# Performance work log

Measured on AMD Instinct MI355X. Metric: run time of the kernel, lower is better.

## Reference

```python
import jax, jax.numpy as jnp
import numpy as np

HIDDEN = 4096
NUM_HEADS = 32
NUM_KV_HEADS = 8
HEAD_DIM = HIDDEN // NUM_HEADS  # 128
Q_SIZE = NUM_HEADS * HEAD_DIM    # 4096
KV_SIZE = NUM_KV_HEADS * HEAD_DIM  # 1024
SCALE = 1.0 / HEAD_DIM  # attention_multiplier=None -> head_dim ** (-1)
ROPE_BASE = 10000.0


def _rope_neox(x, positions):
    # x: [B, S, H, D], positions: [B, S] int
    half = HEAD_DIM // 2
    inv_freq = 1.0 / (ROPE_BASE ** (jnp.arange(0, half, dtype=jnp.float32) / half))
    freqs = positions.astype(jnp.float32)[..., None] * inv_freq  # [B, S, half]
    cos = jnp.cos(freqs)[:, :, None, :]  # [B, S, 1, half]
    sin = jnp.sin(freqs)[:, :, None, :]
    x1, x2 = x[..., :half], x[..., half:]
    return jnp.concatenate([x1 * cos - x2 * sin, x2 * cos + x1 * sin], axis=-1)


def setup_inputs() -> dict:
    key = jax.random.key(0)
    k1, k2, k3 = jax.random.split(key, 3)
    B, S = 2, 2048
    positions = jnp.broadcast_to(jnp.arange(S, dtype=jnp.int32), (B, S))
    hidden_states = jax.random.normal(k1, (B, S, HIDDEN), dtype=jnp.float32) * 0.02
    w_qkv = jax.random.normal(k2, (Q_SIZE + 2 * KV_SIZE, HIDDEN), dtype=jnp.float32) * 0.02
    w_o = jax.random.normal(k3, (HIDDEN, Q_SIZE), dtype=jnp.float32) * 0.02
    return {"positions": positions, "hidden_states": hidden_states, "w_qkv": w_qkv, "w_o": w_o}


def reference(positions, hidden_states, w_qkv, w_o):
    B, S, _ = hidden_states.shape
    # fused QKV projection
    qkv = jnp.einsum('bsh,oh->bso', hidden_states, w_qkv)
    q = qkv[..., :Q_SIZE].reshape(B, S, NUM_HEADS, HEAD_DIM)
    k = qkv[..., Q_SIZE:Q_SIZE + KV_SIZE].reshape(B, S, NUM_KV_HEADS, HEAD_DIM)
    v = qkv[..., Q_SIZE + KV_SIZE:].reshape(B, S, NUM_KV_HEADS, HEAD_DIM)
    # neox-style RoPE on q and k
    q = _rope_neox(q, positions)
    k = _rope_neox(k, positions)
    # GQA: repeat kv heads
    rep = NUM_HEADS // NUM_KV_HEADS
    k = jnp.repeat(k, rep, axis=2)  # [B, S, NUM_HEADS, D]
    v = jnp.repeat(v, rep, axis=2)
    # causal attention
    scores = jnp.einsum('bqhd,bkhd->bhqk', q, k) * SCALE
    causal = jnp.tril(jnp.ones((S, S), dtype=bool))
    scores = jnp.where(causal, scores, jnp.finfo(scores.dtype).min)
    probs = jax.nn.softmax(scores, axis=-1)
    attn = jnp.einsum('bhqk,bkhd->bqhd', probs, v).reshape(B, S, Q_SIZE)
    # output projection
    return jnp.einsum('bsq,hq->bsh', attn, w_o)
```

## Files before the change

kernel.cpp:

```cpp
#include <hip/hip_runtime.h>
#include <hip/hip_bf16.h>
#include <cmath>

typedef __bf16 bf16x8 __attribute__((ext_vector_type(8)));
typedef __bf16 bf16x4 __attribute__((ext_vector_type(4)));
typedef float  f32x4  __attribute__((ext_vector_type(4)));
typedef unsigned int u32;
typedef u32 u32x4 __attribute__((ext_vector_type(4)));

#define AS1 __attribute__((address_space(1)))
#define AS3 __attribute__((address_space(3)))
#define GLDS16(gp, lp) __builtin_amdgcn_global_load_lds((AS1 void*)(gp), (AS3 void*)(lp), 16, 0, 0)

#define B_DIM 2
#define S_LEN 2048
#define HIDDEN 4096
#define NHEADS 32
#define NKV 8
#define HDIM 128
#define QSZ 4096
#define KVSZ 1024
#define QKVSZ 6144
#define GK 4096
#define ATT_SCALE 0.0078125f
#define L2E 1.4426950408889634f

__global__ __launch_bounds__(256) void conv_f32_bf16(const float* __restrict__ in,
                                                     __bf16* __restrict__ out, int n4) {
    int idx = blockIdx.x * 256 + threadIdx.x;
    if (idx < n4) {
        float4 v = ((const float4*)in)[idx];
        bf16x4 o;
        o[0] = (__bf16)v.x; o[1] = (__bf16)v.y; o[2] = (__bf16)v.z; o[3] = (__bf16)v.w;
        ((bf16x4*)out)[idx] = o;
    }
}

__global__ __launch_bounds__(256) void rope_table_kernel(float* __restrict__ ct,
                                                         float* __restrict__ st) {
    int idx = blockIdx.x * 256 + threadIdx.x;
    int p = idx >> 6, i = idx & 63;
    float inv = expf(-(float)i * (9.210340371976184f / 64.0f));
    float freq = (float)p * inv;
    float s, c;
    sincosf(freq, &s, &c);
    ct[idx] = c; st[idx] = s;
}

template<typename OUT>
__global__ __launch_bounds__(512, 2) void gemm256(const __bf16* __restrict__ A,
                                                  const __bf16* __restrict__ B,
                                                  OUT* __restrict__ C,
                                                  int N) {
    __shared__ __bf16 Asm[2 * 16384 + 2 * 16384];
    char* Bbase = (char*)Asm + 65536;

    const int tid = threadIdx.x;
    const int w = tid >> 6, l = tid & 63;
    const int l15 = l & 15, l4 = l >> 4;
    const int wr = w >> 2, wc = w & 3;

    const int nwg = gridDim.x * gridDim.y;
    const int orig = blockIdx.y * gridDim.x + blockIdx.x;
    const int swz = (orig & 7) * (nwg >> 3) + (orig >> 3);
    const int bx = swz % gridDim.x, by = swz / gridDim.x;
    const int m0 = by * 256, n0 = bx * 256;

    const __bf16* Ag = A + (size_t)m0 * GK;
    const __bf16* Bg = B + (size_t)n0 * GK;

#define STAGE_AQ(q, tile) do {                                                  \
        int c_ = (q) * 512 + tid;                                               \
        int r_ = c_ >> 3;                                                       \
        int jg_ = (tid & 7) ^ (r_ & 7);                                         \
        GLDS16(Ag + (size_t)r_ * GK + (tile) * 64 + jg_ * 8,                    \
               (char*)Asm + ((tile) & 1) * 32768 + c_ * 16);                    \
    } while (0)
#define STAGE_BS(s, tile) do {                                                  \
        _Pragma("unroll")                                                       \
        for (int i_ = 0; i_ < 2; ++i_) {                                        \
            int v_ = i_ * 512 + tid;                                            \
            int r_ = (v_ >> 8) * 64 + (s) * 32 + ((v_ >> 3) & 31);              \
            int jg_ = (v_ & 7) ^ (r_ & 7);                                      \
            int c_ = r_ * 8 + (v_ & 7);                                         \
            GLDS16(Bg + (size_t)r_ * GK + (tile) * 64 + jg_ * 8,                \
                   Bbase + ((tile) & 1) * 32768 + c_ * 16);                     \
        }                                                                       \
    } while (0)

#define LOAD_A(DST, MH) do {                                                    \
        _Pragma("unroll")                                                       \
        for (int m2 = 0; m2 < 4; ++m2) {                                        \
            int row = wr * 128 + ((MH) * 4 + m2) * 16 + l15;                    \
            _Pragma("unroll")                                                   \
            for (int kk = 0; kk < 2; ++kk) {                                    \
                int j = (kk * 4 + l4) ^ (row & 7);                              \
                DST[m2][kk] = *(const bf16x8*)(Als + row * 64 + j * 8);         \
            }                                                                   \
        }                                                                       \
    } while (0)
#define LOAD_B(DST, NH) do {                                                    \
        _Pragma("unroll")                                                       \
        for (int n2 = 0; n2 < 2; ++n2) {                                        \
            int row = wc * 64 + ((NH) * 2 + n2) * 16 + l15;                     \
            _Pragma("unroll")                                                   \
            for (int kk = 0; kk < 2; ++kk) {                                    \
                int j = (kk * 4 + l4) ^ (row & 7);                              \
                DST[n2][kk] = *(const bf16x8*)(Bls + row * 64 + j * 8);         \
            }                                                                   \
        }                                                                       \
    } while (0)
#define MFMA_QUAD(AF, BF, MI0, NI0)                                             \
    _Pragma("unroll")                                                           \
    for (int m2 = 0; m2 < 4; ++m2)                                              \
        _Pragma("unroll")                                                       \
        for (int n2 = 0; n2 < 2; ++n2)                                          \
            _Pragma("unroll")                                                   \
            for (int kk = 0; kk < 2; ++kk)                                      \
                acc[(MI0) + m2][(NI0) + n2] =                                   \
                    __builtin_amdgcn_mfma_f32_16x16x32_bf16(                    \
                        AF[m2][kk], BF[n2][kk], acc[(MI0) + m2][(NI0) + n2], 0, 0, 0);
#define PH_SYNC_PRE  do { __builtin_amdgcn_sched_barrier(0);                    \
        __builtin_amdgcn_s_barrier();                                           \
        asm volatile("s_waitcnt lgkmcnt(0)" ::: "memory");                      \
        __builtin_amdgcn_sched_barrier(0); } while (0)
#define PH_SYNC_POST do { __builtin_amdgcn_sched_barrier(0);                    \
        __builtin_amdgcn_s_barrier(); } while (0)

    f32x4 acc[8][4] = {};

    const int T = GK / 64;
    STAGE_AQ(0, 0); STAGE_AQ(1, 0); STAGE_AQ(2, 0); STAGE_AQ(3, 0);
    STAGE_BS(0, 0); STAGE_BS(1, 0);
    STAGE_AQ(0, 1); STAGE_AQ(2, 1); STAGE_BS(0, 1);
    asm volatile("s_waitcnt vmcnt(4)" ::: "memory");
    __builtin_amdgcn_s_barrier();

    for (int t = 0; t < T; ++t) {
        const __bf16* Als = Asm + (t & 1) * 16384;
        const __bf16* Bls = (__bf16*)Bbase + (t & 1) * 16384;
        bf16x8 af0[4][2], af1[4][2], bfr[2][2];
        LOAD_A(af0, 0);
        LOAD_B(bfr, 0);
        if (t + 1 < T) { STAGE_AQ(1, t + 1); STAGE_AQ(3, t + 1); }
        PH_SYNC_PRE;
        __builtin_amdgcn_s_setprio(1);
        MFMA_QUAD(af0, bfr, 0, 0);
        __builtin_amdgcn_s_setprio(0);
        PH_SYNC_POST;
        LOAD_B(bfr, 1);
        if (t + 1 < T) STAGE_BS(1, t + 1);
        PH_SYNC_PRE;
        __builtin_amdgcn_s_setprio(1);
        MFMA_QUAD(af0, bfr, 0, 2);
        __builtin_amdgcn_s_setprio(0);
        PH_SYNC_POST;
        LOAD_A(af1, 1);
        LOAD_B(bfr, 0);
        if (t + 2 < T) { STAGE_AQ(0, t + 2); STAGE_AQ(2, t + 2); }
        PH_SYNC_PRE;
        __builtin_amdgcn_s_setprio(1);
        MFMA_QUAD(af1, bfr, 4, 0);
        __builtin_amdgcn_s_setprio(0);
        PH_SYNC_POST;
        LOAD_B(bfr, 1);
        if (t + 2 < T) STAGE_BS(0, t + 2);
        PH_SYNC_PRE;
        __builtin_amdgcn_s_setprio(1);
        MFMA_QUAD(af1, bfr, 4, 2);
        __builtin_amdgcn_s_setprio(0);
        if (t + 2 < T)      { asm volatile("s_waitcnt vmcnt(4)" ::: "memory"); }
        else if (t + 1 < T) { asm volatile("s_waitcnt vmcnt(0)" ::: "memory"); }
        PH_SYNC_POST;
    }
#undef PH_SYNC_PRE
#undef PH_SYNC_POST
#undef MFMA_QUAD
#undef LOAD_A
#undef LOAD_B
#undef STAGE_AQ
#undef STAGE_BS

#pragma unroll
    for (int mi = 0; mi < 8; ++mi)
#pragma unroll
        for (int ni = 0; ni < 4; ++ni)
#pragma unroll
            for (int r = 0; r < 4; ++r)
                C[(size_t)(m0 + wr * 128 + mi * 16 + l4 * 4 + r) * N
                  + n0 + wc * 64 + ni * 16 + l15] = (OUT)acc[mi][ni][r];
}

__global__ __launch_bounds__(256) void rope_kernel(const __bf16* __restrict__ qkv,
                                                   const int* __restrict__ pos,
                                                   const float* __restrict__ ct,
                                                   const float* __restrict__ st,
                                                   __bf16* __restrict__ Qb,
                                                   __bf16* __restrict__ Kb) {
    const int tid = threadIdx.x;
    const int tok = blockIdx.x;
    const int b = tok >> 11, s = tok & 2047;
    const int p = pos[tok];
    const __bf16* base = qkv + (size_t)tok * QKVSZ;
    const float* cb = ct + (size_t)p * 64;
    const float* sb = st + (size_t)p * 64;
    for (int idx = tid; idx < 2560; idx += 256) {
        int head = idx >> 6, i = idx & 63;
        float c = cb[i], sn = sb[i];
        if (head < 32) {
            float x1 = (float)base[head * HDIM + i];
            float x2 = (float)base[head * HDIM + 64 + i];
            size_t o = ((size_t)(b * 32 + head) * S_LEN + s) * HDIM + i;
            Qb[o]      = (__bf16)((x1 * c - x2 * sn) * ATT_SCALE);
            Qb[o + 64] = (__bf16)((x2 * c + x1 * sn) * ATT_SCALE);
        } else {
            int g = head - 32;
            float x1 = (float)base[QSZ + g * HDIM + i];
            float x2 = (float)base[QSZ + g * HDIM + 64 + i];
            size_t o = ((size_t)(b * 8 + g) * S_LEN + s) * HDIM + i;
            Kb[o]      = (__bf16)(x1 * c - x2 * sn);
            Kb[o + 64] = (__bf16)(x2 * c + x1 * sn);
        }
    }
}

__global__ __launch_bounds__(256) void vtrans_kernel(const __bf16* __restrict__ qkv,
                                                     __bf16* __restrict__ Vt) {
    __shared__ __bf16 T[64][132];
    const int tid = threadIdx.x;
    const int st = blockIdx.x, g = blockIdx.y, b = blockIdx.z;
    const __bf16* src = qkv + ((size_t)(b * S_LEN + st * 64)) * QKVSZ + (QSZ + KVSZ) + g * HDIM;
#pragma unroll
    for (int it = 0; it < 8; ++it) {
        int c = it * 256 + tid;
        int row = c >> 5;
        int c4 = c & 31;
        bf16x4 v = *(const bf16x4*)(src + (size_t)row * QKVSZ + c4 * 4);
        *(bf16x4*)(&T[row][c4 * 4]) = v;
    }
    __syncthreads();
#pragma unroll
    for (int it = 0; it < 8; ++it) {
        int c = it * 256 + tid;
        int d = c >> 4;
        int s4 = (c & 15) * 4;
        bf16x4 o;
        o[0] = T[s4 + 0][d]; o[1] = T[s4 + 1][d]; o[2] = T[s4 + 2][d]; o[3] = T[s4 + 3][d];
        *(bf16x4*)(Vt + ((size_t)(b * 8 + g) * HDIM + d) * S_LEN + st * 64 + s4) = o;
    }
}

__global__ __launch_bounds__(512, 2) void attn_kernel(const __bf16* __restrict__ Q,
                                                      const __bf16* __restrict__ K,
                                                      const __bf16* __restrict__ Vt,
                                                      __bf16* __restrict__ O) {
    const int tid = threadIdx.x;
    const int w = tid >> 6, l = tid & 63;
    const int l15 = l & 15, l4 = l >> 4;
    const int flat = blockIdx.x + (blockIdx.y << 3) + (blockIdx.z << 8);
    const int swz = (flat & 7) * 64 + (flat >> 3);
    const int qt = swz & 7;
    const int hb = swz >> 3;
    const int h = hb & 31, b = hb >> 5;
    const int g = h >> 2;
    const int qw0 = qt * 256 + w * 32;

    __shared__ __bf16 Ks[4][64 * 128];
    __shared__ __bf16 Vs[4][128 * 64];

    const __bf16* Qp = Q + ((size_t)((b * 32 + h) * S_LEN + qw0)) * HDIM;
    const __bf16* Kp = K + (size_t)(b * 8 + g) * S_LEN * HDIM;
    const __bf16* Vp = Vt + (size_t)(b * 8 + g) * HDIM * S_LEN;

    bf16x8 qf[2][4];
#pragma unroll
    for (int qh = 0; qh < 2; ++qh)
#pragma unroll
        for (int kk = 0; kk < 4; ++kk)
            qf[qh][kk] = *(const bf16x8*)(Qp + (size_t)(qh * 16 + l15) * HDIM + kk * 32 + l4 * 8);

    f32x4 acc[2][8] = {};
    float m[2]    = {-1e30f, -1e30f};
    float lsum[2] = {0.f, 0.f};

#define RED16(x, OPINS) do {                                                      \
        u32 ra_ = __builtin_bit_cast(u32, x), rb_;                                \
        asm("v_mov_b32 %0, %1" : "=v"(rb_) : "v"(ra_));                           \
        asm("v_permlane16_swap_b32 %0, %1" : "+v"(ra_), "+v"(rb_));               \
        x = OPINS(__builtin_bit_cast(float, ra_), __builtin_bit_cast(float, rb_));\
    } while (0)
#define RED32(x, OPINS) do {                                                      \
        u32 ra_ = __builtin_bit_cast(u32, x), rb_;                                \
        asm("v_mov_b32 %0, %1" : "=v"(rb_) : "v"(ra_));                           \
        asm("v_permlane32_swap_b32 %0, %1" : "+v"(ra_), "+v"(rb_));               \
        x = OPINS(__builtin_bit_cast(float, ra_), __builtin_bit_cast(float, rb_));\
    } while (0)
#define FADD_(a_, b_) ((a_) + (b_))

#define STAGE(ktile) do {                                                          \
        const int buf_ = (ktile) & 3;                                              \
        const __bf16* kbase = Kp + (size_t)(ktile) * 64 * HDIM;                    \
        _Pragma("unroll")                                                          \
        for (int i_ = 0; i_ < 2; ++i_) {                                           \
            int c_ = i_ * 512 + tid;                \
            int row_ = c_ >> 4, cc_ = (c_ & 15) ^ (row_ & 7);                      \
            GLDS16(kbase + (size_t)row_ * HDIM + cc_ * 8,                          \
                   (char*)Ks[buf_] + c_ * 16);                                     \
        }                                                                          \
        const __bf16* vbase = Vp + (size_t)(ktile) * 64;                           \
        _Pragma("unroll")                                                          \
        for (int i_ = 0; i_ < 2; ++i_) {                                           \
            int c_ = i_ * 512 + tid;                \
            int row_ = c_ >> 3, cc_ = (c_ & 7) ^ (row_ & 7);                       \
            GLDS16(vbase + (size_t)row_ * S_LEN + cc_ * 8,                         \
                   (char*)Vs[buf_] + c_ * 16);                                     \
        }                                                                          \
    } while (0)

    const int nkt = 4 * qt + 4;
    STAGE(0);
    if (1 < nkt) STAGE(1);
    if (2 < nkt) STAGE(2);

    for (int kt = 0; kt < nkt; ++kt) {
        if (kt + 3 < nkt) STAGE(kt + 3);
        {
            int rem = nkt - 1 - kt;
            if (rem >= 3)      { asm volatile("s_waitcnt vmcnt(12)" ::: "memory"); }
            else if (rem == 2) { asm volatile("s_waitcnt vmcnt(8)"  ::: "memory"); }
            else if (rem == 1) { asm volatile("s_waitcnt vmcnt(4)"  ::: "memory"); }
            else               { asm volatile("s_waitcnt vmcnt(0)"  ::: "memory"); }
        }
        __builtin_amdgcn_sched_barrier(0);
        __builtin_amdgcn_s_barrier();
        __builtin_amdgcn_sched_barrier(0);
        const int cur = kt & 3;
        if (kt * 64 <= qw0 + 31) {
            f32x4 sfr[2][4];
            __builtin_amdgcn_s_setprio(1);
#pragma unroll
            for (int fn = 0; fn < 4; ++fn) {
                f32x4 sa0 = {}, sa1 = {};
#pragma unroll
                for (int kk = 0; kk < 4; ++kk) {
                    int row = fn * 16 + l15;
                    int cc = (kk * 4 + l4) ^ (l15 & 7);
                    bf16x8 kb = *(const bf16x8*)(Ks[cur] + row * HDIM + cc * 8);
                    sa0 = __builtin_amdgcn_mfma_f32_16x16x32_bf16(kb, qf[0][kk], sa0, 0, 0, 0);
                    sa1 = __builtin_amdgcn_mfma_f32_16x16x32_bf16(kb, qf[1][kk], sa1, 0, 0, 0);
                }
                sfr[0][fn] = sa0; sfr[1][fn] = sa1;
            }
            __builtin_amdgcn_s_setprio(0);
            const bool needmask = (kt * 64 + 63 > qw0);
            bf16x8 pb[2][2];
#pragma unroll
            for (int qh = 0; qh < 2; ++qh) {
                const int qrow = qw0 + qh * 16 + l15;
                float pmax = -1e30f;
#pragma unroll
                for (int fn = 0; fn < 4; ++fn)
#pragma unroll
                    for (int r = 0; r < 4; ++r) {
                        float v = sfr[qh][fn][r];
                        if (needmask) {
                            int kcol = kt * 64 + fn * 16 + l4 * 4 + r;
                            if (kcol > qrow) v = -1e30f;
                        }
                        sfr[qh][fn][r] = v;
                        pmax = fmaxf(pmax, v);
                    }
                RED16(pmax, fmaxf);
                RED32(pmax, fmaxf);
                if (!__all(pmax - m[qh] <= 8.0f)) {
                    float mn = fmaxf(m[qh], pmax);
                    float alpha = exp2f((m[qh] - mn) * L2E);
                    m[qh] = mn;
                    lsum[qh] *= alpha;
#pragma unroll
                    for (int n = 0; n < 8; ++n)
#pragma unroll
                        for (int r = 0; r < 4; ++r) acc[qh][n][r] *= alpha;
                }
                float rs = 0.f;
                u32 pk01[4], pk23[4];
#pragma unroll
                for (int fn = 0; fn < 4; ++fn) {
                    float p0 = exp2f((sfr[qh][fn][0] - m[qh]) * L2E);
                    float p1 = exp2f((sfr[qh][fn][1] - m[qh]) * L2E);
                    float p2 = exp2f((sfr[qh][fn][2] - m[qh]) * L2E);
                    float p3 = exp2f((sfr[qh][fn][3] - m[qh]) * L2E);
                    rs += (p0 + p1) + (p2 + p3);
                    asm("v_cvt_pk_bf16_f32 %0, %1, %2" : "=v"(pk01[fn]) : "v"(p0), "v"(p1));
                    asm("v_cvt_pk_bf16_f32 %0, %1, %2" : "=v"(pk23[fn]) : "v"(p2), "v"(p3));
                }
                RED16(rs, FADD_);
                RED32(rs, FADD_);
                lsum[qh] += rs;
#pragma unroll
                for (int kk = 0; kk < 2; ++kk) {
                    u32 w0 = pk01[2 * kk], w2 = pk01[2 * kk + 1];
                    asm("v_permlane32_swap_b32 %0, %1" : "+v"(w0), "+v"(w2));
                    asm("v_permlane16_swap_b32 %0, %1" : "+v"(w0), "+v"(w2));
                    u32 w1 = pk23[2 * kk], w3 = pk23[2 * kk + 1];
                    asm("v_permlane32_swap_b32 %0, %1" : "+v"(w1), "+v"(w3));
                    asm("v_permlane16_swap_b32 %0, %1" : "+v"(w1), "+v"(w3));
                    u32x4 wv;
                    wv[0] = w0; wv[1] = w1; wv[2] = w2; wv[3] = w3;
                    pb[qh][kk] = __builtin_bit_cast(bf16x8, wv);
                }
            }
            __builtin_amdgcn_s_setprio(1);
#pragma unroll
            for (int kk = 0; kk < 2; ++kk) {
#pragma unroll
                for (int n = 0; n < 8; ++n) {
                    int row = n * 16 + l15;
                    int cc = (kk * 4 + l4) ^ (l15 & 7);
                    bf16x8 vb = *(const bf16x8*)(Vs[cur] + row * 64 + cc * 8);
                    acc[0][n] = __builtin_amdgcn_mfma_f32_16x16x32_bf16(vb, pb[0][kk], acc[0][n], 0, 0, 0);
                    acc[1][n] = __builtin_amdgcn_mfma_f32_16x16x32_bf16(vb, pb[1][kk], acc[1][n], 0, 0, 0);
                }
            }
            __builtin_amdgcn_s_setprio(0);
        }
        __builtin_amdgcn_sched_barrier(0);
        __builtin_amdgcn_s_barrier();
        __builtin_amdgcn_sched_barrier(0);
    }
#undef STAGE
#undef RED16
#undef RED32
#undef FADD_
#pragma unroll
    for (int qh = 0; qh < 2; ++qh) {
        float inv = 1.0f / lsum[qh];
        int qrow = qw0 + qh * 16 + l15;
        __bf16* obase = O + ((size_t)(b * S_LEN) + qrow) * QSZ + h * HDIM + l4 * 4;
#pragma unroll
        for (int n = 0; n < 8; ++n) {
            bf16x4 o4;
#pragma unroll
            for (int r = 0; r < 4; ++r) o4[r] = (__bf16)(acc[qh][n][r] * inv);
            *(bf16x4*)(obase + n * 16) = o4;
        }
    }
}

extern "C" void kernel_launch(void* const* d_in, const int* in_sizes, int n_in,
                              void* d_out, int out_size, void* d_ws, size_t ws_size,
                              hipStream_t stream) {
    const int*   pos    = (const int*)d_in[0];
    const float* hidden = (const float*)d_in[1];
    const float* wqkv   = (const float*)d_in[2];
    const float* wo     = (const float*)d_in[3];
    float* out = (float*)d_out;

    __bf16* hb    = (__bf16*)d_ws;
    __bf16* wqb   = hb  + 16777216;
    __bf16* wob   = wqb + 25165824;
    __bf16* qkv   = wob + 16777216;
    __bf16* Qb    = qkv + 25165824;
    __bf16* Kb    = Qb  + 16777216;
    __bf16* Vtb   = Kb  + 4194304;
    __bf16* attnb = Vtb + 4194304;
    float*  rc    = (float*)(attnb + 16777216);
    float*  rs    = rc + 131072;

    conv_f32_bf16<<<16384, 256, 0, stream>>>(hidden, hb, 4194304);
    conv_f32_bf16<<<24576, 256, 0, stream>>>(wqkv, wqb, 6291456);
    conv_f32_bf16<<<16384, 256, 0, stream>>>(wo, wob, 4194304);
    rope_table_kernel<<<512, 256, 0, stream>>>(rc, rs);
    gemm256<__bf16><<<dim3(QKVSZ / 256, (B_DIM * S_LEN) / 256), 512, 0, stream>>>(hb, wqb, qkv, QKVSZ);
    rope_kernel<<<B_DIM * S_LEN, 256, 0, stream>>>(qkv, pos, rc, rs, Qb, Kb);
    vtrans_kernel<<<dim3(S_LEN / 64, NKV, B_DIM), 256, 0, stream>>>(qkv, Vtb);
    attn_kernel<<<dim3(S_LEN / 256, NHEADS, B_DIM), 512, 0, stream>>>(Qb, Kb, Vtb, attnb);
    gemm256<float><<<dim3(HIDDEN / 256, (B_DIM * S_LEN) / 256), 512, 0, stream>>>(attnb, wob, out, HIDDEN);
}
```

Measured before the change: 620.0 us.

## Add dedicated 128x384-tile QKV GEMM kernel to improve CU occupancy balance

Replaces the generic 256x256-tile GEMM for the QKV projection with a specialized kernel using 128x384 tiles, so the grid is 512 workgroups, matching two blocks per CU. The inner loop splits each K-step into three MFMA phases over the B sub-tiles, with barriers and priority hints between them. The aim is to remove partial-wave tail imbalance. In exchange, the smaller M tile lowers data reuse per tile and adds more barriers.

```diff
diff --git a/kernel.cpp b/kernel.cpp
--- a/kernel.cpp
+++ b/kernel.cpp
@@ -45,6 +45,133 @@
     float s, c;
     sincosf(freq, &s, &c);
     ct[idx] = c; st[idx] = s;
+}
+
+__global__ __launch_bounds__(512, 2) void gemm_qkv(const __bf16* __restrict__ A,
+                                                   const __bf16* __restrict__ B,
+                                                   __bf16* __restrict__ C) {
+    __shared__ __bf16 Asm[2 * 8192];
+    __shared__ __bf16 Bsm[2 * 24576];
+
+    const int tid = threadIdx.x;
+    const int w = tid >> 6, l = tid & 63;
+    const int l15 = l & 15, l4 = l >> 4;
+    const int wr = w >> 2, wc = w & 3;
+
+    const int nwg = gridDim.x * gridDim.y;
+    const int orig = blockIdx.y * gridDim.x + blockIdx.x;
+    const int swz = (orig & 7) * (nwg >> 3) + (orig >> 3);
+    const int bx = swz % gridDim.x, by = swz / gridDim.x;
+    const int m0 = by * 128, n0 = bx * 384;
+
+    const __bf16* Ag = A + (size_t)m0 * GK;
+    const __bf16* Bg = B + (size_t)n0 * GK;
+
+#define QSTAGE_ALL(tile) do {                                                   \
+        _Pragma("unroll")                                                       \
+        for (int i_ = 0; i_ < 2; ++i_) {           \
+            int c_ = i_ * 512 + tid;                                            \
+            int r_ = c_ >> 3;                                                   \
+            int jg_ = (c_ & 7) ^ (r_ & 7);                                      \
+            GLDS16(Ag + (size_t)r_ * GK + (tile) * 64 + jg_ * 8,                \
+                   (char*)Asm + ((tile) & 1) * 16384 + c_ * 16);                \
+        }                                                                       \
+        _Pragma("unroll")                                                       \
+        for (int i_ = 0; i_ < 6; ++i_) {           \
+            int c_ = i_ * 512 + tid;                                            \
+            int r_ = c_ >> 3;                                                   \
+            int jg_ = (c_ & 7) ^ (r_ & 7);                                      \
+            GLDS16(Bg + (size_t)r_ * GK + (tile) * 64 + jg_ * 8,                \
+                   (char*)Bsm + ((tile) & 1) * 49152 + c_ * 16);                \
+        }                                                                       \
+    } while (0)
+
+#define QLOAD_A(DST) do {                                                       \
+        _Pragma("unroll")                                                       \
+        for (int m2 = 0; m2 < 4; ++m2) {                                        \
+            int row = wr * 64 + m2 * 16 + l15;                                  \
+            _Pragma("unroll")                                                   \
+            for (int kk = 0; kk < 2; ++kk) {                                    \
+                int j = (kk * 4 + l4) ^ (row & 7);                              \
+                DST[m2][kk] = *(const bf16x8*)(Als + row * 64 + j * 8);         \
+            }                                                                   \
+        }                                                                       \
+    } while (0)
+#define QLOAD_B(DST, NH) do {                                                   \
+        _Pragma("unroll")                                                       \
+        for (int n2 = 0; n2 < 2; ++n2) {                                        \
+            int row = wc * 96 + ((NH) * 2 + n2) * 16 + l15;                     \
+            _Pragma("unroll")                                                   \
+            for (int kk = 0; kk < 2; ++kk) {                                    \
+                int j = (kk * 4 + l4) ^ (row & 7);                              \
+                DST[n2][kk] = *(const bf16x8*)(Bls + row * 64 + j * 8);         \
+            }                                                                   \
+        }                                                                       \
+    } while (0)
+#define QMFMA(AF, BF, NI0)                                                      \
+    _Pragma("unroll")                                                           \
+    for (int m2 = 0; m2 < 4; ++m2)                                              \
+        _Pragma("unroll")                                                       \
+        for (int n2 = 0; n2 < 2; ++n2)                                          \
+            _Pragma("unroll")                                                   \
+            for (int kk = 0; kk < 2; ++kk)                                      \
+                acc[m2][(NI0) + n2] = __builtin_amdgcn_mfma_f32_16x16x32_bf16(  \
+                    AF[m2][kk], BF[n2][kk], acc[m2][(NI0) + n2], 0, 0, 0);
+#define QSYNC_PRE  do { __builtin_amdgcn_sched_barrier(0);                      \
+        __builtin_amdgcn_s_barrier();                                           \
+        asm volatile("s_waitcnt lgkmcnt(0)" ::: "memory");                      \
+        __builtin_amdgcn_sched_barrier(0); } while (0)
+#define QSYNC_POST do { __builtin_amdgcn_sched_barrier(0);                      \
+        __builtin_amdgcn_s_barrier(); } while (0)
+
+    f32x4 acc[4][6] = {};
+
+    const int T = GK / 64;
+    QSTAGE_ALL(0);
+    asm volatile("s_waitcnt vmcnt(0)" ::: "memory");
+    __builtin_amdgcn_s_barrier();
+
+    for (int t = 0; t < T; ++t) {
+        const __bf16* Als = Asm + (t & 1) * 8192;
+        const __bf16* Bls = Bsm + (t & 1) * 24576;
+        bf16x8 af[4][2], bfr[2][2];
+        QLOAD_A(af);
+        QLOAD_B(bfr, 0);
+        if (t + 1 < T) QSTAGE_ALL(t + 1);
+        QSYNC_PRE;
+        __builtin_amdgcn_s_setprio(1);
+        QMFMA(af, bfr, 0);
+        __builtin_amdgcn_s_setprio(0);
+        QSYNC_POST;
+        QLOAD_B(bfr, 1);
+        QSYNC_PRE;
+        __builtin_amdgcn_s_setprio(1);
+        QMFMA(af, bfr, 2);
+        __builtin_amdgcn_s_setprio(0);
+        QSYNC_POST;
+        QLOAD_B(bfr, 2);
+        QSYNC_PRE;
+        __builtin_amdgcn_s_setprio(1);
+        QMFMA(af, bfr, 4);
+        __builtin_amdgcn_s_setprio(0);
+        if (t + 1 < T) { asm volatile("s_waitcnt vmcnt(0)" ::: "memory"); }
+        QSYNC_POST;
+    }
+#undef QSYNC_PRE
+#undef QSYNC_POST
+#undef QMFMA
+#undef QLOAD_A
+#undef QLOAD_B
+#undef QSTAGE_ALL
+
+#pragma unroll
+    for (int mi = 0; mi < 4; ++mi)
+#pragma unroll
+        for (int ni = 0; ni < 6; ++ni)
+#pragma unroll
+            for (int r = 0; r < 4; ++r)
+                C[(size_t)(m0 + wr * 64 + mi * 16 + l4 * 4 + r) * QKVSZ
+                  + n0 + wc * 96 + ni * 16 + l15] = (__bf16)acc[mi][ni][r];
 }
 
 template<typename OUT>
@@ -471,7 +598,7 @@
     conv_f32_bf16<<<24576, 256, 0, stream>>>(wqkv, wqb, 6291456);
     conv_f32_bf16<<<16384, 256, 0, stream>>>(wo, wob, 4194304);
     rope_table_kernel<<<512, 256, 0, stream>>>(rc, rs);
-    gemm256<__bf16><<<dim3(QKVSZ / 256, (B_DIM * S_LEN) / 256), 512, 0, stream>>>(hb, wqb, qkv, QKVSZ);
+    gemm_qkv<<<dim3(QKVSZ / 384, (B_DIM * S_LEN) / 128), 512, 0, stream>>>(hb, wqb, qkv);
     rope_kernel<<<B_DIM * S_LEN, 256, 0, stream>>>(qkv, pos, rc, rs, Qb, Kb);
     vtrans_kernel<<<dim3(S_LEN / 64, NKV, B_DIM), 256, 0, stream>>>(qkv, Vtb);
     attn_kernel<<<dim3(S_LEN / 256, NHEADS, B_DIM), 512, 0, stream>>>(Qb, Kb, Vtb, attnb);
```

Result: slower. 668.3 us (+7.8%).
